# Optimization experiments

Hardware: AMD Instinct MI355X
Metric: run time of the kernel (lower is better)

## Reference

```python
import jax, jax.numpy as jnp
import numpy as np


def _l2norm(t, axis=-1, eps=1e-12):
    # matches torch F.normalize: x / max(||x||, eps)
    n = jnp.sqrt(jnp.sum(t * t, axis=axis, keepdims=True))
    return t / jnp.maximum(n, eps)


def setup_inputs() -> dict:
    key = jax.random.key(0)
    ks = jax.random.split(key, 5)
    B, N, C, H = 16, 4096, 768, 12
    x = jax.random.normal(ks[0], (B, N, C), dtype=jnp.float32)
    Wqkv = jax.random.normal(ks[1], (C, 3 * C), dtype=jnp.float32) * (C ** -0.5)
    bqkv = jax.random.normal(ks[2], (3 * C,), dtype=jnp.float32) * 0.02
    Wproj = jax.random.normal(ks[3], (C, C), dtype=jnp.float32) * (C ** -0.5)
    bproj = jax.random.normal(ks[4], (C,), dtype=jnp.float32) * 0.02
    temperature = jnp.ones((H, 1, 1), dtype=jnp.float32)
    return {"x": x, "Wqkv": Wqkv, "bqkv": bqkv, "Wproj": Wproj,
            "bproj": bproj, "temperature": temperature}


def reference(x, Wqkv, bqkv, Wproj, bproj, temperature):
    B, N, C = x.shape
    H = temperature.shape[0]
    Dh = C // H
    qkv = x @ Wqkv + bqkv                      # [B,N,3C]
    qkv = qkv.reshape(B, N, 3, H, Dh)
    # -> [3,B,H,Dh,N] (channels-as-tokens layout)
    qkv = jnp.transpose(qkv, (2, 0, 3, 4, 1))
    q, k, v = qkv[0], qkv[1], qkv[2]           # each [B,H,Dh,N]
    q = _l2norm(q, axis=-1)
    k = _l2norm(k, axis=-1)
    # cross-covariance over channels: [B,H,Dh,Dh]
    attn = jnp.einsum('bhdn,bhen->bhde', q, k) * temperature
    attn = jax.nn.softmax(attn, axis=-1)
    out = jnp.einsum('bhde,bhen->bhdn', attn, v)  # [B,H,Dh,N]
    out = jnp.transpose(out, (0, 3, 1, 2)).reshape(B, N, C)
    return out @ Wproj + bproj
```

## Files before the change

kernel.cpp:

```cpp
#include <hip/hip_runtime.h>

typedef __bf16 bf16x8 __attribute__((ext_vector_type(8)));
typedef float  f32x4  __attribute__((ext_vector_type(4)));
typedef unsigned short u16x8 __attribute__((ext_vector_type(8)));
typedef unsigned short u16x4 __attribute__((ext_vector_type(4)));

#define MFMA16(a, b, c) __builtin_amdgcn_mfma_f32_16x16x32_bf16((a), (b), (c), 0, 0, 0)

#define GLOAD16(g, l) __builtin_amdgcn_global_load_lds( \
    (const __attribute__((address_space(1))) void*)(g),  \
    (__attribute__((address_space(3))) void*)(l), 16, 0, 0)

__device__ __forceinline__ float bf2f(unsigned short u) {
    unsigned int x = ((unsigned int)u) << 16;
    return __builtin_bit_cast(float, x);
}
__device__ __forceinline__ unsigned short f2bf(float f) {
    unsigned int x = __builtin_bit_cast(unsigned int, f);
    x = x + 0x7FFFu + ((x >> 16) & 1u);
    return (unsigned short)(x >> 16);
}
__device__ __forceinline__ bool is_f32(const unsigned short* tf) { return tf[0] == 0; }
__device__ __forceinline__ float ldscal(const void* p, int i, bool f32m) {
    return f32m ? ((const float*)p)[i] : bf2f(((const unsigned short*)p)[i]);
}

__global__ __launch_bounds__(256)
void tr_dual(const void* __restrict__ in_, unsigned short* __restrict__ xb,
             unsigned short* __restrict__ xbT, float* __restrict__ sB,
             const unsigned short* __restrict__ tf)
{
    __shared__ unsigned short T[64 * 72];
    const bool f32m = is_f32(tf);
    const int tx = blockIdx.x % 12;
    const int ty = blockIdx.x / 12;
    const int r0 = ty * 64, c0 = tx * 64;
    const int t = threadIdx.x;
#pragma unroll
    for (int s = 0; s < 2; ++s) {
        const int idx = t + s * 256;
        const int rr = idx >> 3;
        const int cc = (idx & 7) * 8;
        u16x8 v;
        if (f32m) {
            const float* inf = (const float*)in_;
            f32x4 a = *(const f32x4*)&inf[(size_t)(r0 + rr) * 768 + c0 + cc];
            f32x4 b = *(const f32x4*)&inf[(size_t)(r0 + rr) * 768 + c0 + cc + 4];
#pragma unroll
            for (int j = 0; j < 4; ++j) { v[j] = f2bf(a[j]); v[4 + j] = f2bf(b[j]); }
        } else {
            v = *(const u16x8*)&((const unsigned short*)in_)[(size_t)(r0 + rr) * 768 + c0 + cc];
        }
        *(u16x8*)&xb[(size_t)(r0 + rr) * 768 + c0 + cc] = v;
#pragma unroll
        for (int j = 0; j < 8; ++j) T[(cc + j) * 72 + rr] = v[j];
    }
    __syncthreads();
#pragma unroll
    for (int s = 0; s < 2; ++s) {
        const int idx = t + s * 256;
        const int cc = idx >> 3;
        const int rr = (idx & 7) * 8;
        u16x8 v = *(const u16x8*)&T[cc * 72 + rr];
        *(u16x8*)&xbT[(size_t)(c0 + cc) * 65536 + r0 + rr] = v;
    }
    {
        const int col = t >> 2;
        const int seg = t & 3;
        float s = 0.f;
#pragma unroll
        for (int r = 0; r < 16; ++r) s += bf2f(T[col * 72 + seg * 16 + r]);
        s += __shfl_xor(s, 1);
        s += __shfl_xor(s, 2);
        if (seg == 0) atomicAdd(&sB[(r0 >> 12) * 768 + c0 + col], s);
    }
}

__device__ __forceinline__ void tr_tile(const void* in_, unsigned short* out,
                                        int R, int C, int istride,
                                        int bid, bool f32m, unsigned short* T)
{
    const int nct = C >> 6;
    const int tx = bid % nct;
    const int ty = bid / nct;
    const int r0 = ty * 64, c0 = tx * 64;
    const int t = threadIdx.x;
#pragma unroll
    for (int s = 0; s < 2; ++s) {
        const int idx = t + s * 256;
        const int rr = idx >> 3;
        const int cc = (idx & 7) * 8;
        unsigned short v[8];
        if (f32m) {
            const float* inf = (const float*)in_;
            f32x4 a = *(const f32x4*)&inf[(size_t)(r0 + rr) * istride + c0 + cc];
            f32x4 b = *(const f32x4*)&inf[(size_t)(r0 + rr) * istride + c0 + cc + 4];
#pragma unroll
            for (int j = 0; j < 4; ++j) { v[j] = f2bf(a[j]); v[4 + j] = f2bf(b[j]); }
        } else {
            u16x8 a = *(const u16x8*)&((const unsigned short*)in_)[(size_t)(r0 + rr) * istride + c0 + cc];
#pragma unroll
            for (int j = 0; j < 8; ++j) v[j] = a[j];
        }
#pragma unroll
        for (int j = 0; j < 8; ++j) T[(cc + j) * 72 + rr] = v[j];
    }
    __syncthreads();
#pragma unroll
    for (int s = 0; s < 2; ++s) {
        const int idx = t + s * 256;
        const int cc = idx >> 3;
        const int rr = (idx & 7) * 8;
        u16x8 v = *(const u16x8*)&T[cc * 72 + rr];
        *(u16x8*)&out[(size_t)(c0 + cc) * R + r0 + rr] = v;
    }
}

__global__ __launch_bounds__(256)
void wprep(const void* __restrict__ Wqkv, const void* __restrict__ Wp,
           unsigned short* __restrict__ WqkT, unsigned short* __restrict__ Wv_bf,
           unsigned short* __restrict__ WprojT, const unsigned short* __restrict__ tf)
{
    __shared__ unsigned short T[64 * 72];
    const bool f32m = is_f32(tf);
    const int bid = blockIdx.x;
    if (bid < 288) {
        tr_tile(Wqkv, WqkT, 768, 1536, 2304, bid, f32m, T);
    } else if (bid < 576) {
        const int t = (bid - 288) * 256 + threadIdx.x;
        const int c = t / 96;
        const int e0 = (t % 96) * 8;
        u16x8 v;
        if (f32m) {
            const float* p = (const float*)Wqkv + (size_t)c * 2304 + 1536 + e0;
            f32x4 a = *(const f32x4*)p;
            f32x4 b = *(const f32x4*)(p + 4);
#pragma unroll
            for (int j = 0; j < 4; ++j) { v[j] = f2bf(a[j]); v[4 + j] = f2bf(b[j]); }
        } else {
            v = *(const u16x8*)&((const unsigned short*)Wqkv)[(size_t)c * 2304 + 1536 + e0];
        }
        *(u16x8*)&Wv_bf[(size_t)c * 768 + e0] = v;
    } else {
        tr_tile(Wp, WprojT, 768, 768, 768, bid - 576, f32m, T);
    }
}

__global__ __launch_bounds__(256, 2)
void gemmG(const unsigned short* __restrict__ A, unsigned short* __restrict__ G)
{
    constexpr int NT = 64;
    constexpr size_t LD = 65536;
    __shared__ __align__(16) char SM[65536];
    unsigned short* lds = (unsigned short*)SM;

    const int tid  = threadIdx.x;
    const int wave = tid >> 6;
    const int lane = tid & 63;
    const int wm   = wave >> 1;
    const int wn   = wave & 1;
    const int lr   = lane & 15;
    const int lq   = lane >> 4;

    const int per = gridDim.x >> 3;
    const int wg  = (blockIdx.x & 7) * per + (blockIdx.x >> 3);
    const int b = wg / 36;
    const int r36 = wg % 36;
    const int mt = r36 / 6, nt = r36 % 6;
    const size_t m0 = (size_t)mt * 128;
    const int n0 = nt * 128;

    const unsigned short* Ab = A + m0 * LD + (size_t)b * 4096;
    const unsigned short* Bb = A + (size_t)n0 * LD + (size_t)b * 4096;

    f32x4 zero = {0.f, 0.f, 0.f, 0.f};
    f32x4 acc[4][4];
#pragma unroll
    for (int i = 0; i < 4; ++i)
#pragma unroll
        for (int j = 0; j < 4; ++j) acc[i][j] = zero;

    auto STAGE = [&](int t) {
        unsigned short* la_ = lds + (t & 1) * 16384;
        unsigned short* lb_ = la_ + 8192;
#pragma unroll
        for (int it = 0; it < 4; ++it) {
            const int c = it * 256 + tid;
            const int row = c >> 3;
            const int gs = (c & 7) ^ (row & 7);
            GLOAD16(Ab + (size_t)row * LD + t * 64 + gs * 8, la_ + c * 8);
        }
#pragma unroll
        for (int it = 0; it < 4; ++it) {
            const int c = it * 256 + tid;
            const int row = c >> 3;
            const int gs = (c & 7) ^ (row & 7);
            GLOAD16(Bb + (size_t)row * LD + t * 64 + gs * 8, lb_ + c * 8);
        }
    };

    STAGE(0);
    STAGE(1);

    for (int t = 0; t < NT; ++t) {
        if (t + 1 < NT) asm volatile("s_waitcnt vmcnt(8)" ::: "memory");
        else            asm volatile("s_waitcnt vmcnt(0)" ::: "memory");
        __builtin_amdgcn_s_barrier();
        __builtin_amdgcn_sched_barrier(0);

        const char* la = (const char*)(lds + (t & 1) * 16384);
        const char* lb = la + 16384;

        bf16x8 bfr[4][2], af[4][2];
#pragma unroll
        for (int ni = 0; ni < 4; ++ni)
#pragma unroll
            for (int ks = 0; ks < 2; ++ks) {
                const int row = wn * 64 + ni * 16 + lr;
                const int s   = ks * 4 + lq;
                bfr[ni][ks] = *(const bf16x8*)(lb + row * 128 + ((s ^ (row & 7)) << 4));
            }
#pragma unroll
        for (int mi = 0; mi < 4; ++mi)
#pragma unroll
            for (int ks = 0; ks < 2; ++ks) {
                const int row = wm * 64 + mi * 16 + lr;
                const int s   = ks * 4 + lq;
                af[mi][ks] = *(const bf16x8*)(la + row * 128 + ((s ^ (row & 7)) << 4));
            }
        __builtin_amdgcn_s_setprio(1);
#pragma unroll
        for (int mi = 0; mi < 4; ++mi)
#pragma unroll
            for (int ni = 0; ni < 4; ++ni)
#pragma unroll
                for (int ks = 0; ks < 2; ++ks)
                    acc[mi][ni] = MFMA16(af[mi][ks], bfr[ni][ks], acc[mi][ni]);
        __builtin_amdgcn_s_setprio(0);

        __builtin_amdgcn_sched_barrier(0);
        __builtin_amdgcn_s_barrier();
        if (t + 2 < NT) STAGE(t + 2);
    }

#pragma unroll
    for (int mi = 0; mi < 4; ++mi)
#pragma unroll
        for (int ni = 0; ni < 4; ++ni)
#pragma unroll
            for (int r = 0; r < 4; ++r) {
                const size_t row = m0 + (size_t)(wm * 64 + mi * 16 + lq * 4 + r);
                const int col = n0 + wn * 64 + ni * 16 + lr;
                G[(size_t)b * 589824 + row * 768 + col] = f2bf(acc[mi][ni][r]);
            }
}

template<int MODE>
__global__ __launch_bounds__(512, 4)
void gemmH(const unsigned short* __restrict__ A,
           const unsigned short* __restrict__ BT,
           const float* __restrict__ bias,
           unsigned short* __restrict__ o0,
           float* __restrict__ oF,
           const unsigned short* __restrict__ tf)
{
    constexpr int K = 768, NT = 24;
    __shared__ __align__(16) char SM[49152];

    const bool f32m = is_f32(tf);
    const int tid  = threadIdx.x;
    const int wave = tid >> 6;
    const int lane = tid & 63;
    const int wm   = wave >> 2;
    const int wn   = wave & 3;
    const int lr   = lane & 15;
    const int lq   = lane >> 4;

    const int per = gridDim.x >> 3;
    const int wg  = (blockIdx.x & 7) * per + (blockIdx.x >> 3);
    int b = 0, mt, nt;
    if (MODE == 4) { b = wg / 36; const int r = wg % 36; mt = r / 3; nt = r % 3; }
    else           { mt = wg / 3; nt = wg % 3; }
    const size_t m0 = (size_t)mt * 128;
    const int n0 = nt * 256;

    const unsigned short* Ab = A + m0 * K;
    const unsigned short* Bb;
    if (MODE == 1)      Bb = BT + (m0 >> 12) * (size_t)589824 + (size_t)n0 * K;
    else if (MODE == 4) Bb = BT + (size_t)b * 589824 + (size_t)n0 * K;
    else                Bb = BT + (size_t)n0 * K;

    f32x4 zero = {0.f, 0.f, 0.f, 0.f};
    f32x4 acc[4][4];
#pragma unroll
    for (int i = 0; i < 4; ++i)
#pragma unroll
        for (int j = 0; j < 4; ++j) acc[i][j] = zero;

    auto STAGE = [&](int t) {
        char* base = SM + (t & 1) * 24576;
        {
            const int c = tid;
            const int rp = c >> 3;
            const int ch = (c & 7) ^ (rp & 7);
            const int srow = rp * 2 + (ch >> 2);
            const int sk = (ch & 3) * 8;
            GLOAD16(Ab + (size_t)srow * K + t * 32 + sk, base + c * 16);
        }
#pragma unroll
        for (int ev = 0; ev < 2; ++ev) {
            const int c = ev * 512 + tid;
            const int rp = c >> 3;
            const int ch = (c & 7) ^ (rp & 7);
            const int srow = rp * 2 + (ch >> 2);
            const int sk = (ch & 3) * 8;
            GLOAD16(Bb + (size_t)srow * K + t * 32 + sk, base + 8192 + c * 16);
        }
    };

    STAGE(0);
    STAGE(1);

    for (int t = 0; t < NT; ++t) {
        if (t + 1 < NT) asm volatile("s_waitcnt vmcnt(3)" ::: "memory");
        else            asm volatile("s_waitcnt vmcnt(0)" ::: "memory");
        __builtin_amdgcn_s_barrier();
        __builtin_amdgcn_sched_barrier(0);

        const char* la = SM + (t & 1) * 24576;
        const char* lb = la + 8192;

        bf16x8 af[4], bfr[4];
#pragma unroll
        for (int ni = 0; ni < 4; ++ni) {
            const int row = wn * 64 + ni * 16 + lr;
            const int rp = row >> 1;
            const int ch = (row & 1) * 4 + lq;
            bfr[ni] = *(const bf16x8*)(lb + rp * 128 + ((ch ^ (rp & 7)) << 4));
        }
#pragma unroll
        for (int mi = 0; mi < 4; ++mi) {
            const int row = wm * 64 + mi * 16 + lr;
            const int rp = row >> 1;
            const int ch = (row & 1) * 4 + lq;
            af[mi] = *(const bf16x8*)(la + rp * 128 + ((ch ^ (rp & 7)) << 4));
        }
        __builtin_amdgcn_s_setprio(1);
#pragma unroll
        for (int mi = 0; mi < 4; ++mi)
#pragma unroll
            for (int ni = 0; ni < 4; ++ni)
                acc[mi][ni] = MFMA16(af[mi], bfr[ni], acc[mi][ni]);
        __builtin_amdgcn_s_setprio(0);

        __builtin_amdgcn_sched_barrier(0);
        __builtin_amdgcn_s_barrier();
        if (t + 2 < NT) STAGE(t + 2);
    }

    float bb[4];
#pragma unroll
    for (int ni = 0; ni < 4; ++ni) {
        const int col = n0 + wn * 64 + ni * 16 + lr;
        bb[ni] = (MODE == 1) ? bias[(m0 >> 12) * 768 + col] : 0.f;
    }

#pragma unroll
    for (int mi = 0; mi < 4; ++mi)
#pragma unroll
        for (int ni = 0; ni < 4; ++ni)
#pragma unroll
            for (int r = 0; r < 4; ++r) {
                const size_t row = m0 + (size_t)(wm * 64 + mi * 16 + lq * 4 + r);
                const int col = n0 + wn * 64 + ni * 16 + lr;
                const float val = acc[mi][ni][r] + bb[ni];
                if (MODE == 1) {
                    if (f32m) oF[row * 768 + col] = val;
                    else      o0[row * 768 + col] = f2bf(val);
                } else if (MODE == 2) {
                    o0[row * 768 + col] = f2bf(val);
                } else {
                    o0[(size_t)b * 1179648 + row * 768 + col] = f2bf(val);
                }
            }
}

__global__ __launch_bounds__(256)
void attn2(const unsigned short* __restrict__ P,
           const unsigned short* __restrict__ WqkT,
           const float* __restrict__ s,
           const void* __restrict__ bqkv,
           const unsigned short* __restrict__ tf,
           unsigned short* __restrict__ attnT)
{
    __shared__ float S[64][64];
    __shared__ float nq[64], nk[64], uq[64], uk[64];
    __shared__ float sb[768];
    __shared__ float bkv[64];
    const bool f32m = is_f32(tf);
    const int bh = blockIdx.x;
    const int b = bh / 12, h = bh % 12;
    const unsigned short* Pq = P + (size_t)b * 1179648 + (size_t)(h * 64) * 768;
    const unsigned short* Pk = Pq + 768 * 768;
    const unsigned short* Wq = WqkT + (size_t)(h * 64) * 768;
    const unsigned short* Wk = Wq + 768 * 768;
    const int tid = threadIdx.x;
    const int wave = tid >> 6;
    const int lane = tid & 63;
    const int lr = lane & 15;
    const int lq = lane >> 4;

    for (int i = tid; i < 768; i += 256) sb[i] = s[b * 768 + i];
    if (tid < 64) bkv[tid] = ldscal(bqkv, 768 + h * 64 + tid, f32m);

    f32x4 zero = {0.f, 0.f, 0.f, 0.f};
    f32x4 acc[4][4];
#pragma unroll
    for (int i = 0; i < 4; ++i)
#pragma unroll
        for (int j = 0; j < 4; ++j) acc[i][j] = zero;

    for (int ks = 0; ks < 6; ++ks) {
        const int j0 = wave * 192 + ks * 32 + lq * 8;
        u16x8 qa[4], ka[4];
#pragma unroll
        for (int mi = 0; mi < 4; ++mi)
            qa[mi] = *(const u16x8*)&Pq[(size_t)(mi * 16 + lr) * 768 + j0];
#pragma unroll
        for (int ni = 0; ni < 4; ++ni)
            ka[ni] = *(const u16x8*)&Wk[(size_t)(ni * 16 + lr) * 768 + j0];
#pragma unroll
        for (int mi = 0; mi < 4; ++mi)
#pragma unroll
            for (int ni = 0; ni < 4; ++ni)
                acc[mi][ni] = MFMA16(__builtin_bit_cast(bf16x8, qa[mi]),
                                     __builtin_bit_cast(bf16x8, ka[ni]),
                                     acc[mi][ni]);
    }
    __syncthreads();

    for (int ww = 0; ww < 4; ++ww) {
        if (wave == ww) {
#pragma unroll
            for (int mi = 0; mi < 4; ++mi)
#pragma unroll
                for (int ni = 0; ni < 4; ++ni)
#pragma unroll
                    for (int r = 0; r < 4; ++r) {
                        const int d = mi * 16 + lq * 4 + r;
                        const int e = ni * 16 + lr;
                        if (ww == 0) S[d][e] = acc[mi][ni][r];
                        else         S[d][e] += acc[mi][ni][r];
                    }
        }
        __syncthreads();
    }

    const int d  = tid >> 2;
    const int q4 = tid & 3;
    {
        const unsigned short* pqr = Pq + (size_t)d * 768 + q4 * 192;
        const unsigned short* wqr = Wq + (size_t)d * 768 + q4 * 192;
        const unsigned short* pkr = Pk + (size_t)d * 768 + q4 * 192;
        const unsigned short* wkr = Wk + (size_t)d * 768 + q4 * 192;
        float a_nq = 0.f, a_uq = 0.f, a_nk = 0.f, a_uk = 0.f;
        for (int i = 0; i < 24; ++i) {
            u16x8 vp = *(const u16x8*)&pqr[i * 8];
            u16x8 vw = *(const u16x8*)&wqr[i * 8];
            u16x8 kp = *(const u16x8*)&pkr[i * 8];
            u16x8 kw = *(const u16x8*)&wkr[i * 8];
#pragma unroll
            for (int j = 0; j < 8; ++j) {
                const float wqv = bf2f(vw[j]);
                const float wkv = bf2f(kw[j]);
                const float sj = sb[q4 * 192 + i * 8 + j];
                a_nq += bf2f(vp[j]) * wqv;
                a_uq += sj * wqv;
                a_nk += bf2f(kp[j]) * wkv;
                a_uk += sj * wkv;
            }
        }
        a_nq += __shfl_xor(a_nq, 1); a_nq += __shfl_xor(a_nq, 2);
        a_uq += __shfl_xor(a_uq, 1); a_uq += __shfl_xor(a_uq, 2);
        a_nk += __shfl_xor(a_nk, 1); a_nk += __shfl_xor(a_nk, 2);
        a_uk += __shfl_xor(a_uk, 1); a_uk += __shfl_xor(a_uk, 2);
        if (q4 == 0) { nq[d] = a_nq; uq[d] = a_uq; nk[d] = a_nk; uk[d] = a_uk; }
    }
    __syncthreads();

    const float tv  = f32m ? ((const float*)tf)[h] : bf2f(tf[h]);
    const float bqd = ldscal(bqkv, h * 64 + d, f32m);
    const float uqd = uq[d];
    const float nqf = nq[d] + 2.f * bqd * uqd + 4096.f * bqd * bqd;
    const float qn  = fmaxf(sqrtf(fmaxf(nqf, 0.f)), 1e-12f);
    float vals[16];
    float mx = -1e30f;
#pragma unroll
    for (int i = 0; i < 16; ++i) {
        const int e = q4 * 16 + i;
        const float bke = bkv[e];
        const float nkf = nk[e] + 2.f * bke * uk[e] + 4096.f * bke * bke;
        const float kn  = fmaxf(sqrtf(fmaxf(nkf, 0.f)), 1e-12f);
        const float sv  = S[d][e] + bqd * uk[e] + uqd * bke + 4096.f * bqd * bke;
        const float val = sv / (qn * kn) * tv;
        vals[i] = val;
        mx = fmaxf(mx, val);
    }
    mx = fmaxf(mx, __shfl_xor(mx, 1));
    mx = fmaxf(mx, __shfl_xor(mx, 2));
    float sum = 0.f;
#pragma unroll
    for (int i = 0; i < 16; ++i) { vals[i] = __expf(vals[i] - mx); sum += vals[i]; }
    sum += __shfl_xor(sum, 1);
    sum += __shfl_xor(sum, 2);
    const float inv = 1.0f / sum;
#pragma unroll
    for (int i = 0; i < 16; ++i) {
        const int e = q4 * 16 + i;
        attnT[(size_t)bh * 4096 + e * 64 + d] = f2bf(vals[i] * inv);
    }
}

__global__ __launch_bounds__(512)
void mb_build(const unsigned short* __restrict__ attnT,
              const unsigned short* __restrict__ WprojT,
              unsigned short* __restrict__ MbT)
{
    const int bh = blockIdx.x;
    const int b = bh / 12, h = bh % 12;
    const int tid = threadIdx.x;
    const int wave = tid >> 6;
    const int lane = tid & 63;
    const unsigned short* At = attnT + (size_t)bh * 4096;

    f32x4 zero = {0.f, 0.f, 0.f, 0.f};
    f32x4 acc[4][6];
#pragma unroll
    for (int i = 0; i < 4; ++i)
#pragma unroll
        for (int j = 0; j < 6; ++j) acc[i][j] = zero;

    const int lr  = lane & 15;
    const int lk8 = (lane >> 4) * 8;

#pragma unroll
    for (int ks = 0; ks < 2; ++ks) {
        bf16x8 af[4], bfr[6];
#pragma unroll
        for (int mi = 0; mi < 4; ++mi)
            af[mi] = *(const bf16x8*)&At[(mi * 16 + lr) * 64 + ks * 32 + lk8];
#pragma unroll
        for (int ni = 0; ni < 6; ++ni) {
            const int j = wave * 96 + ni * 16 + lr;
            bfr[ni] = *(const bf16x8*)&WprojT[(size_t)j * 768 + h * 64 + ks * 32 + lk8];
        }
#pragma unroll
        for (int mi = 0; mi < 4; ++mi)
#pragma unroll
            for (int ni = 0; ni < 6; ++ni)
                acc[mi][ni] = MFMA16(af[mi], bfr[ni], acc[mi][ni]);
    }

#pragma unroll
    for (int mi = 0; mi < 4; ++mi)
#pragma unroll
        for (int ni = 0; ni < 6; ++ni) {
            const int e = mi * 16 + (lane >> 4) * 4;
            const int j = wave * 96 + ni * 16 + lr;
            u16x4 pk;
#pragma unroll
            for (int r = 0; r < 4; ++r) pk[r] = f2bf(acc[mi][ni][r]);
            *(u16x4*)&MbT[(size_t)b * 589824 + (size_t)j * 768 + h * 64 + e] = pk;
        }
}

__global__ __launch_bounds__(256)
void beff_k(const unsigned short* __restrict__ MbT,
            const void* __restrict__ bqkv, const void* __restrict__ bp,
            float* __restrict__ beff, const unsigned short* __restrict__ tf)
{
    __shared__ float bv[768];
    const bool f32m = is_f32(tf);
    for (int i = threadIdx.x; i < 768; i += 256) bv[i] = ldscal(bqkv, 1536 + i, f32m);
    __syncthreads();
    const int t = blockIdx.x * 256 + threadIdx.x;
    const int b = t / 768, j = t % 768;
    float s = ldscal(bp, j, f32m);
    const unsigned short* row = MbT + (size_t)b * 589824 + (size_t)j * 768;
    for (int e8 = 0; e8 < 96; ++e8) {
        u16x8 m = *(const u16x8*)&row[e8 * 8];
#pragma unroll
        for (int jj = 0; jj < 8; ++jj) s += bf2f(m[jj]) * bv[e8 * 8 + jj];
    }
    beff[t] = s;
}

extern "C" void kernel_launch(void* const* d_in, const int* in_sizes, int n_in,
                              void* d_out, int out_size, void* d_ws, size_t ws_size,
                              hipStream_t stream)
{
    const void* x    = d_in[0];
    const void* Wqkv = d_in[1];
    const void* bqkv = d_in[2];
    const void* Wp   = d_in[3];
    const void* bp   = d_in[4];
    const unsigned short* tf = (const unsigned short*)d_in[5];

    char* w = (char*)d_ws;
    unsigned short* xbT    = (unsigned short*)(w);
    unsigned short* xb     = (unsigned short*)(w + 100663296);
    unsigned short* G      = (unsigned short*)(w + 201326592);
    unsigned short* P      = (unsigned short*)(w + 220200960);
    unsigned short* PT     = (unsigned short*)(w + 257949696);
    unsigned short* MbT    = (unsigned short*)(w + 276824064);
    unsigned short* WqkT   = (unsigned short*)(w + 295698432);
    unsigned short* Wv_bf  = (unsigned short*)(w + 298057728);
    unsigned short* WprojT = (unsigned short*)(w + 299237376);
    unsigned short* attnT  = (unsigned short*)(w + 300417024);
    float*          sB     = (float*)(w + 301989888);
    float*          beff   = (float*)(w + 302039040);

    hipMemsetAsync(sB, 0, 16 * 768 * sizeof(float), stream);
    tr_dual<<<dim3(12288), dim3(256), 0, stream>>>(x, xb, xbT, sB, tf);
    wprep<<<dim3(720), dim3(256), 0, stream>>>(Wqkv, Wp, WqkT, Wv_bf, WprojT, tf);

    gemmG<<<dim3(576), dim3(256), 0, stream>>>(xbT, G);
    gemmH<4><<<dim3(576), dim3(512), 0, stream>>>(WqkT, G, nullptr, P, nullptr, tf);
    attn2<<<dim3(192), dim3(256), 0, stream>>>(P, WqkT, sB, bqkv, tf, attnT);
    mb_build<<<dim3(192), dim3(512), 0, stream>>>(attnT, WprojT, MbT);
    gemmH<2><<<dim3(288), dim3(512), 0, stream>>>(MbT, Wv_bf, nullptr, PT, nullptr, tf);
    beff_k<<<dim3(48), dim3(256), 0, stream>>>(MbT, bqkv, bp, beff, tf);
    gemmH<1><<<dim3(1536), dim3(512), 0, stream>>>(xb, PT, beff,
        (unsigned short*)d_out, (float*)d_out, tf);
}
```

Measured before the change: 445.0 us.

## Exploit Gram symmetry in gemmG and triple-buffer gemmH LDS pipeline

After: 422.8 us. -5.0%, faster.

```diff
diff --git a/kernel.cpp b/kernel.cpp
--- a/kernel.cpp
+++ b/kernel.cpp
@@ -164,14 +164,17 @@
 
     const int per = gridDim.x >> 3;
     const int wg  = (blockIdx.x & 7) * per + (blockIdx.x >> 3);
-    const int b = wg / 36;
-    const int r36 = wg % 36;
-    const int mt = r36 / 6, nt = r36 % 6;
+    const int b = wg / 21;
+    int rr21 = wg % 21;
+    int mt = 0;
+    while (rr21 >= 6 - mt) { rr21 -= 6 - mt; ++mt; }
+    const int nt = mt + rr21;
     const size_t m0 = (size_t)mt * 128;
     const int n0 = nt * 128;
 
     const unsigned short* Ab = A + m0 * LD + (size_t)b * 4096;
     const unsigned short* Bb = A + (size_t)n0 * LD + (size_t)b * 4096;
+    unsigned short* Gb = G + (size_t)b * 589824;
 
     f32x4 zero = {0.f, 0.f, 0.f, 0.f};
     f32x4 acc[4][4];
@@ -251,8 +254,33 @@
             for (int r = 0; r < 4; ++r) {
                 const size_t row = m0 + (size_t)(wm * 64 + mi * 16 + lq * 4 + r);
                 const int col = n0 + wn * 64 + ni * 16 + lr;
-                G[(size_t)b * 589824 + row * 768 + col] = f2bf(acc[mi][ni][r]);
+                Gb[row * 768 + col] = f2bf(acc[mi][ni][r]);
             }
+
+    if (mt != nt) {
+        asm volatile("s_waitcnt lgkmcnt(0)" ::: "memory");
+        __builtin_amdgcn_s_barrier();
+        unsigned short* CTw = (unsigned short*)SM + wave * (64 * 68);
+#pragma unroll
+        for (int mi = 0; mi < 4; ++mi)
+#pragma unroll
+            for (int ni = 0; ni < 4; ++ni) {
+                u16x4 pk;
+#pragma unroll
+                for (int r = 0; r < 4; ++r) pk[r] = f2bf(acc[mi][ni][r]);
+                *(u16x4*)&CTw[(ni * 16 + lr) * 68 + mi * 16 + lq * 4] = pk;
+            }
+#pragma unroll
+        for (int rep = 0; rep < 8; ++rep) {
+            const int idx = rep * 64 + lane;
+            const int c = idx >> 3;
+            const int j = (idx & 7) * 8;
+            u16x8 v = *(const u16x8*)&CTw[c * 68 + j];
+            const size_t rowT = (size_t)n0 + wn * 64 + c;
+            const int colT = (int)m0 + wm * 64 + j;
+            *(u16x8*)&Gb[rowT * 768 + colT] = v;
+        }
+    }
 }
 
 template<int MODE>
@@ -265,7 +293,7 @@
            const unsigned short* __restrict__ tf)
 {
     constexpr int K = 768, NT = 24;
-    __shared__ __align__(16) char SM[49152];
+    __shared__ __align__(16) char SM[73728];
 
     const bool f32m = is_f32(tf);
     const int tid  = threadIdx.x;
@@ -298,7 +326,7 @@
         for (int j = 0; j < 4; ++j) acc[i][j] = zero;
 
     auto STAGE = [&](int t) {
-        char* base = SM + (t & 1) * 24576;
+        char* base = SM + (t % 3) * 24576;
         {
             const int c = tid;
             const int rp = c >> 3;
@@ -320,14 +348,16 @@
 
     STAGE(0);
     STAGE(1);
+    STAGE(2);
 
     for (int t = 0; t < NT; ++t) {
-        if (t + 1 < NT) asm volatile("s_waitcnt vmcnt(3)" ::: "memory");
-        else            asm volatile("s_waitcnt vmcnt(0)" ::: "memory");
+        if (t + 2 < NT)      asm volatile("s_waitcnt vmcnt(6)" ::: "memory");
+        else if (t + 1 < NT) asm volatile("s_waitcnt vmcnt(3)" ::: "memory");
+        else                 asm volatile("s_waitcnt vmcnt(0)" ::: "memory");
         __builtin_amdgcn_s_barrier();
         __builtin_amdgcn_sched_barrier(0);
 
-        const char* la = SM + (t & 1) * 24576;
+        const char* la = SM + (t % 3) * 24576;
         const char* lb = la + 8192;
 
         bf16x8 af[4], bfr[4];
@@ -355,7 +385,7 @@
 
         __builtin_amdgcn_sched_barrier(0);
         __builtin_amdgcn_s_barrier();
-        if (t + 2 < NT) STAGE(t + 2);
+        if (t + 3 < NT) STAGE(t + 3);
     }
 
     float bb[4];
@@ -624,12 +654,12 @@
     tr_dual<<<dim3(12288), dim3(256), 0, stream>>>(x, xb, xbT, sB, tf);
     wprep<<<dim3(720), dim3(256), 0, stream>>>(Wqkv, Wp, WqkT, Wv_bf, WprojT, tf);
 
-    gemmG<<<dim3(576), dim3(256), 0, stream>>>(xbT, G);
+    gemmG<<<dim3(336), dim3(256), 0, stream>>>(xbT, G);
     gemmH<4><<<dim3(576), dim3(512), 0, stream>>>(WqkT, G, nullptr, P, nullptr, tf);
     attn2<<<dim3(192), dim3(256), 0, stream>>>(P, WqkT, sB, bqkv, tf, attnT);
     mb_build<<<dim3(192), dim3(512), 0, stream>>>(attnT, WprojT, MbT);
+    beff_k<<<dim3(48), dim3(256), 0, stream>>>(MbT, bqkv, bp, beff, tf);
     gemmH<2><<<dim3(288), dim3(512), 0, stream>>>(MbT, Wv_bf, nullptr, PT, nullptr, tf);
-    beff_k<<<dim3(48), dim3(256), 0, stream>>>(MbT, bqkv, bp, beff, tf);
     gemmH<1><<<dim3(1536), dim3(512), 0, stream>>>(xb, PT, beff,
         (unsigned short*)d_out, (float*)d_out, tf);
 }
```
